# Optimization experiments

Measured on AMD Instinct MI355X. Metric: run time of the kernel, lower is better.

Reference implementation:

```python
import jax, jax.numpy as jnp
import numpy as np

CE_TEMP = 1.0
SIMW_TEMP = 0.1
NSEG = 2048
EPS = 1e-8
NEG = jnp.float32(-1e30)


def setup_inputs() -> dict:
    key = jax.random.key(0)
    k1, k2, k3, k4, k5, k6 = jax.random.split(key, 6)
    N, C, H, W, Ch, S = 2, 19, 128, 128, 256, NSEG
    inputs_plbl = jax.random.normal(k1, (N, C, H, W), dtype=jnp.float32)
    feats_plbl = jax.random.normal(k2, (N, Ch, H, W), dtype=jnp.float32)
    inputs = jax.random.normal(k3, (N, C, H, W), dtype=jnp.float32)
    # multi-hot targets per superpixel; ~2.3 active classes on average -> many multi-hot rows
    targets = jax.random.bernoulli(k4, 0.12, (N, S, C)).astype(jnp.float32)
    superpixels = jax.random.randint(k5, (N, H, W), 0, S, dtype=jnp.int32)
    spmasks = jax.random.bernoulli(k6, 0.5, (N, H, W))
    return {"inputs_plbl": inputs_plbl, "feats_plbl": feats_plbl, "inputs": inputs,
            "targets": targets, "superpixels": superpixels, "spmasks": spmasks}


def _per_image(out_plbl, feat, out, trg_table, sp, mask):
    # out_plbl: [HW,C] softmax'd pseudo-label probs; feat: [HW,Ch]; out: [HW,C];
    # trg_table: [S,C] multi-hot; sp: [HW] int superpixel ids; mask: [HW] bool
    HW, C = out_plbl.shape
    S = trg_table.shape[0]
    trg_pix = trg_table[sp]                                  # [HW,C]
    multi_spx = trg_table.sum(-1) > 1.0                      # [S]
    valid = mask & multi_spx[sp]                             # == spmask & multi-hot mask

    # scatter_max: argmax pixel per (superpixel, class) among valid pixels
    scores = jnp.where(valid[:, None], out_plbl, NEG)
    seg_max = jax.ops.segment_max(scores, sp, num_segments=S)       # [S,C]
    is_max = valid[:, None] & (scores >= seg_max[sp])
    cand = jnp.where(is_max, jnp.arange(HW, dtype=jnp.int32)[:, None], HW)
    proto_idx = jax.ops.segment_min(cand, sp, num_segments=S)       # [S,C]
    proto_idx = jnp.clip(proto_idx, 0, HW - 1)

    # prototype features and per-pixel similarities to own-superpixel class prototypes
    proto_feat = feat[proto_idx]                             # [S,C,Ch]
    pf_pix = proto_feat[sp]                                  # [HW,C,Ch] (dominant intermediate)
    sim = jnp.einsum('kcd,kd->kc', pf_pix, feat) / SIMW_TEMP  # [HW,C]

    # scatter_softmax over the active classes of the pixel's superpixel
    active = trg_pix > 0.0
    w_multi = jax.nn.softmax(jnp.where(active, sim, NEG), axis=-1)
    w_row = jnp.where(active, w_multi, trg_pix)              # inactive entries keep 0
    w = jnp.where(valid[:, None], w_row, trg_pix)            # non-multi pixels keep one-hot
    w = jax.lax.stop_gradient(w)                             # original computes weights under no_grad

    ce = -jnp.log(out + EPS)                                 # [HW,C]
    contrib = jnp.where(mask[:, None], w * ce, 0.0)
    any_valid = jnp.any(valid)                               # image skipped if no multi-hot masked pixel
    loss_i = jnp.where(any_valid, contrib.sum(), 0.0)
    cnt_i = jnp.where(any_valid, mask.sum(), 0)
    return loss_i, cnt_i


def reference(inputs_plbl, feats_plbl, inputs, targets, superpixels, spmasks):
    N, C, H, W = inputs_plbl.shape
    Ch = feats_plbl.shape[1]
    out_plbl = jax.nn.softmax(inputs_plbl / CE_TEMP, axis=1).transpose(0, 2, 3, 1).reshape(N, -1, C)
    feats = feats_plbl.transpose(0, 2, 3, 1).reshape(N, -1, Ch)
    out = jax.nn.softmax(inputs / CE_TEMP, axis=1).transpose(0, 2, 3, 1).reshape(N, -1, C)
    sp = superpixels.reshape(N, -1)
    mask = spmasks.reshape(N, -1)
    loss_i, cnt_i = jax.vmap(_per_image)(out_plbl, feats, out, targets, sp, mask)
    total = loss_i.sum()
    cnt = cnt_i.sum()
    return jnp.where(cnt > 0, total / jnp.maximum(cnt, 1).astype(jnp.float32), 0.0)
```

## Files before the change

kernel.cpp:

```cpp
#include <hip/hip_runtime.h>
#include <cstdint>
#include <cstddef>

#define NN   2
#define CC   19
#define HWD  16384
#define CH   256
#define SS   2048
#define BCAP 32

#define EPSV 1e-8f

__global__ __launch_bounds__(256) void k_main(
        const float* __restrict__ xp, const float* __restrict__ xi,
        const float* __restrict__ trg, const int* __restrict__ sp,
        const int* __restrict__ msk,
        int* __restrict__ sp_cnt, unsigned short* __restrict__ bucket,
        unsigned char* __restrict__ validf, float* __restrict__ plbl_pm,
        float* __restrict__ ce_pm, int* __restrict__ cnt,
        int* __restrict__ vcnt, float* __restrict__ slots) {
    int gid = blockIdx.x * blockDim.x + threadIdx.x;
    int partB = (gid >= NN * HWD);
    int idx = partB ? gid - NN * HWD : gid;
    int n = idx >> 14;
    int k = idx & (HWD - 1);
    int lane = threadIdx.x & 63;
    int m = (msk[idx] != 0);
    int s = sp[idx];
    const float* t = trg + ((size_t)n * SS + s) * CC;
    int mu = 0;
    if (m) {
        float ts = 0.f;
        #pragma unroll
        for (int c = 0; c < CC; ++c) ts += t[c];
        mu = (ts > 1.0f);
    }
    int valid = m && mu;

    if (!partB) {
        validf[idx] = (unsigned char)valid;
        unsigned long long mb = __ballot(m);
        unsigned long long vb = __ballot(valid);
        if (valid) {
            int cell = n * SS + s;
            int pos = atomicAdd(&sp_cnt[cell], 1);
            if (pos < BCAP) bucket[(size_t)cell * BCAP + pos] = (unsigned short)k;
            const float* a = xp + (size_t)n * CC * HWD + k;
            float v[CC];
            float mx = -1e30f;
            #pragma unroll
            for (int c = 0; c < CC; ++c) { v[c] = a[(size_t)c * HWD]; mx = fmaxf(mx, v[c]); }
            float su = 0.f;
            #pragma unroll
            for (int c = 0; c < CC; ++c) { v[c] = expf(v[c] - mx); su += v[c]; }
            float inv = 1.f / su;
            float* op = plbl_pm + (size_t)idx * CC;
            #pragma unroll
            for (int c = 0; c < CC; ++c) op[c] = v[c] * inv;
        }
        if (lane == 0) {
            if (mb) atomicAdd(&cnt[n], __popcll(mb));
            if (vb) atomicAdd(&vcnt[n], __popcll(vb));
        }
    } else {
        float contrib = 0.f;
        if (m) {
            const float* b = xi + (size_t)n * CC * HWD + k;
            float v[CC];
            float mx = -1e30f;
            #pragma unroll
            for (int c = 0; c < CC; ++c) { v[c] = b[(size_t)c * HWD]; mx = fmaxf(mx, v[c]); }
            float su = 0.f;
            #pragma unroll
            for (int c = 0; c < CC; ++c) { v[c] = expf(v[c] - mx); su += v[c]; }
            float inv = 1.f / su;
            if (mu) {
                float* cp = ce_pm + (size_t)idx * CC;
                #pragma unroll
                for (int c = 0; c < CC; ++c) cp[c] = -logf(v[c] * inv + EPSV);
            } else {
                #pragma unroll
                for (int c = 0; c < CC; ++c) contrib += t[c] * (-logf(v[c] * inv + EPSV));
            }
        }
        #pragma unroll
        for (int off = 32; off >= 1; off >>= 1) contrib += __shfl_xor(contrib, off);
        if (lane == 0 && contrib != 0.f)
            atomicAdd(&slots[n * 128 + ((idx >> 6) & 127)], contrib);
    }
}

__global__ void k_transpose(const float* __restrict__ F,
                            const unsigned char* __restrict__ validf,
                            float* __restrict__ FT) {
    __shared__ float tile[64][65];
    __shared__ unsigned char vld[64];
    int n  = blockIdx.z;
    int k0 = blockIdx.x * 64;
    int d0 = blockIdx.y * 64;
    const float* src = F + (size_t)n * CH * HWD;
    float* dst = FT + (size_t)n * HWD * CH;
    int tx = threadIdx.x, ty = threadIdx.y;
    if (ty == 0) vld[tx] = validf[n * HWD + k0 + tx];
    #pragma unroll
    for (int i = 0; i < 16; ++i) {
        int dd = ty + 4 * i;
        tile[dd][tx] = src[(size_t)(d0 + dd) * HWD + (k0 + tx)];
    }
    __syncthreads();
    #pragma unroll
    for (int i = 0; i < 16; ++i) {
        int kk = ty + 4 * i;
        if (vld[kk]) dst[(size_t)(k0 + kk) * CH + (d0 + tx)] = tile[tx][kk];
    }
}

__global__ __launch_bounds__(256) void k_sim(
        const float* __restrict__ feat_t, const float* __restrict__ ce_pm,
        const float* __restrict__ plbl_pm, const float* __restrict__ trg,
        const int* __restrict__ sp_cnt, const unsigned short* __restrict__ bucket,
        float* __restrict__ slots) {
    int id = blockIdx.x;
    int cnt_c = sp_cnt[id];
    if (cnt_c == 0) return;
    cnt_c = min(cnt_c, BCAP);
    int n    = id >> 11;
    int tid  = threadIdx.x;
    int lane = tid & 63;
    int wv   = tid >> 6;

    __shared__ float protoF[CC][CH];
    __shared__ float s_bv[4][CC];
    __shared__ int   s_bi[4][CC];
    __shared__ int   s_proto[CC];
    __shared__ int   actc[CC];

    float t = (lane < CC) ? trg[(size_t)id * CC + lane] : 0.f;
    unsigned long long act = __ballot(t > 0.f);
    int nact = __popcll(act);
    int apos = __popcll(act & ((1ull << lane) - 1ull));
    if ((act >> lane) & 1ull) actc[apos] = lane;
    int mypix = (lane < cnt_c) ? (int)bucket[(size_t)id * BCAP + lane] : 0;

    float bv = -1e30f;
    int   bi = HWD;
    for (int i = wv; i < cnt_c; i += 4) {
        int pix = __shfl(mypix, i);
        if (lane < CC) {
            float v = plbl_pm[((size_t)(n * HWD + pix)) * CC + lane];
            if (v > bv || (v == bv && pix < bi)) { bv = v; bi = pix; }
        }
    }
    if (lane < CC) { s_bv[wv][lane] = bv; s_bi[wv][lane] = bi; }
    __syncthreads();
    if (lane < CC) {
        bv = -1e30f; bi = HWD;
        #pragma unroll
        for (int j = 0; j < 4; ++j) {
            float v = s_bv[j][lane];
            int   p = s_bi[j][lane];
            if (v > bv || (v == bv && p < bi)) { bv = v; bi = p; }
        }
        if ((act >> lane) & 1ull) s_proto[apos] = bi;
    }
    __syncthreads();

    for (int a = wv; a < nact; a += 4) {
        int p = s_proto[a];
        ((float4*)(&protoF[a][0]))[lane] =
            ((const float4*)(feat_t + ((size_t)(n * HWD + p)) * CH))[lane];
    }
    __syncthreads();

    float wcontrib = 0.f;
    for (int i = wv; i < cnt_c; i += 4) {
        int pix = __shfl(mypix, i);
        float ce = (lane < nact)
                 ? ce_pm[((size_t)(n * HWD + pix)) * CC + actc[lane]] : 0.f;
        float4 f = ((const float4*)(feat_t + ((size_t)(n * HWD + pix)) * CH))[lane];
        float mysim = -1e30f;
        for (int a = 0; a < nact; ++a) {
            float4 pf = ((const float4*)(&protoF[a][0]))[lane];
            float d = f.x * pf.x + f.y * pf.y + f.z * pf.z + f.w * pf.w;
            #pragma unroll
            for (int off = 32; off >= 1; off >>= 1) d += __shfl_xor(d, off);
            if (lane == a) mysim = d * 10.0f;
        }
        float mx = mysim;
        #pragma unroll
        for (int off = 32; off >= 1; off >>= 1) mx = fmaxf(mx, __shfl_xor(mx, off));
        float e = (lane < nact) ? expf(mysim - mx) : 0.f;
        float se = e;
        #pragma unroll
        for (int off = 32; off >= 1; off >>= 1) se += __shfl_xor(se, off);
        float c1 = (e / se) * ce;
        #pragma unroll
        for (int off = 32; off >= 1; off >>= 1) c1 += __shfl_xor(c1, off);
        wcontrib += c1;
    }
    if (lane == 0 && wcontrib != 0.f)
        atomicAdd(&slots[n * 128 + (id & 127)], wcontrib);
}

__global__ void k_final(const float* __restrict__ slots, const int* __restrict__ cnt,
                        const int* __restrict__ vcnt, float* __restrict__ out) {
    __shared__ float red[2];
    int t = threadIdx.x;
    int w = t >> 6;
    int lane = t & 63;
    float v = slots[w * 128 + lane] + slots[w * 128 + lane + 64];
    #pragma unroll
    for (int off = 32; off >= 1; off >>= 1) v += __shfl_xor(v, off);
    if (lane == 0) red[w] = v;
    __syncthreads();
    if (t == 0) {
        float total = 0.f;
        int c = 0;
        for (int n = 0; n < NN; ++n)
            if (vcnt[n] > 0) { total += red[n]; c += cnt[n]; }
        out[0] = (c > 0) ? total / (float)c : 0.f;
    }
}

extern "C" void kernel_launch(void* const* d_in, const int* in_sizes, int n_in,
                              void* d_out, int out_size, void* d_ws, size_t ws_size,
                              hipStream_t stream) {
    const float* inputs_plbl = (const float*)d_in[0];
    const float* feats_plbl  = (const float*)d_in[1];
    const float* inputs      = (const float*)d_in[2];
    const float* targets     = (const float*)d_in[3];
    const int*   superpixels = (const int*)d_in[4];
    const int*   spmasks     = (const int*)d_in[5];
    float* out = (float*)d_out;

    char* ws = (char*)d_ws;
    int*   sp_cnt = (int*)ws;
    int*   cnt    = (int*)(ws + 16384);
    int*   vcnt   = (int*)(ws + 16392);
    float* slots  = (float*)(ws + 16416);
    unsigned char*  validf = (unsigned char*)(ws + 17440);
    unsigned short* bucket = (unsigned short*)(ws + 50208);
    float* plbl_pm = (float*)(ws + 312352);
    float* ce_pm   = (float*)(ws + 2802720);
    float* feat_t  = (float*)(ws + 5293088);

    hipMemsetAsync(ws, 0, 17440, stream);

    k_main<<<(2 * NN * HWD) / 256, 256, 0, stream>>>(
        inputs_plbl, inputs, targets, superpixels, spmasks,
        sp_cnt, bucket, validf, plbl_pm, ce_pm, cnt, vcnt, slots);
    dim3 tg(HWD / 64, CH / 64, NN);
    k_transpose<<<tg, dim3(64, 4), 0, stream>>>(feats_plbl, validf, feat_t);
    k_sim<<<NN * SS, 256, 0, stream>>>(feat_t, ce_pm, plbl_pm, targets,
                                       sp_cnt, bucket, slots);
    k_final<<<1, 128, 0, stream>>>(slots, cnt, vcnt, out);
}
```

Baseline: 133.4 us.

## Fuse pixel softmax kernel and feature transpose into one launch

Merges the per-pixel softmax/CE kernel and the masked feature transpose into a single kernel, with blocks partitioned by blockIdx. The transpose blocks now recompute the valid flag from mask, superpixel and target sums, so the validf buffer is gone. This removes one launch and the serial dependency between the two kernels, letting the transpose run alongside the softmax work. The cost is redundant target-row reads in the transpose blocks and a shared-memory tile that every block reserves, including the softmax blocks that never use it.

```diff
diff --git a/kernel.cpp b/kernel.cpp
--- a/kernel.cpp
+++ b/kernel.cpp
@@ -11,107 +11,123 @@
 
 #define EPSV 1e-8f
 
-__global__ __launch_bounds__(256) void k_main(
+#define MAIN_BLKS  (2 * NN * HWD / 256)
+#define TRAN_BLKS  ((HWD / 64) * (CH / 64) * NN)
+
+__global__ __launch_bounds__(256) void k_fused(
         const float* __restrict__ xp, const float* __restrict__ xi,
-        const float* __restrict__ trg, const int* __restrict__ sp,
-        const int* __restrict__ msk,
+        const float* __restrict__ F, const float* __restrict__ trg,
+        const int* __restrict__ sp, const int* __restrict__ msk,
         int* __restrict__ sp_cnt, unsigned short* __restrict__ bucket,
-        unsigned char* __restrict__ validf, float* __restrict__ plbl_pm,
-        float* __restrict__ ce_pm, int* __restrict__ cnt,
+        float* __restrict__ plbl_pm, float* __restrict__ ce_pm,
+        float* __restrict__ feat_t, int* __restrict__ cnt,
         int* __restrict__ vcnt, float* __restrict__ slots) {
-    int gid = blockIdx.x * blockDim.x + threadIdx.x;
-    int partB = (gid >= NN * HWD);
-    int idx = partB ? gid - NN * HWD : gid;
-    int n = idx >> 14;
-    int k = idx & (HWD - 1);
-    int lane = threadIdx.x & 63;
-    int m = (msk[idx] != 0);
-    int s = sp[idx];
-    const float* t = trg + ((size_t)n * SS + s) * CC;
-    int mu = 0;
-    if (m) {
-        float ts = 0.f;
-        #pragma unroll
-        for (int c = 0; c < CC; ++c) ts += t[c];
-        mu = (ts > 1.0f);
-    }
-    int valid = m && mu;
-
-    if (!partB) {
-        validf[idx] = (unsigned char)valid;
-        unsigned long long mb = __ballot(m);
-        unsigned long long vb = __ballot(valid);
-        if (valid) {
-            int cell = n * SS + s;
-            int pos = atomicAdd(&sp_cnt[cell], 1);
-            if (pos < BCAP) bucket[(size_t)cell * BCAP + pos] = (unsigned short)k;
-            const float* a = xp + (size_t)n * CC * HWD + k;
-            float v[CC];
-            float mx = -1e30f;
-            #pragma unroll
-            for (int c = 0; c < CC; ++c) { v[c] = a[(size_t)c * HWD]; mx = fmaxf(mx, v[c]); }
-            float su = 0.f;
-            #pragma unroll
-            for (int c = 0; c < CC; ++c) { v[c] = expf(v[c] - mx); su += v[c]; }
-            float inv = 1.f / su;
-            float* op = plbl_pm + (size_t)idx * CC;
-            #pragma unroll
-            for (int c = 0; c < CC; ++c) op[c] = v[c] * inv;
-        }
-        if (lane == 0) {
-            if (mb) atomicAdd(&cnt[n], __popcll(mb));
-            if (vb) atomicAdd(&vcnt[n], __popcll(vb));
-        }
-    } else {
-        float contrib = 0.f;
-        if (m) {
-            const float* b = xi + (size_t)n * CC * HWD + k;
-            float v[CC];
-            float mx = -1e30f;
-            #pragma unroll
-            for (int c = 0; c < CC; ++c) { v[c] = b[(size_t)c * HWD]; mx = fmaxf(mx, v[c]); }
-            float su = 0.f;
-            #pragma unroll
-            for (int c = 0; c < CC; ++c) { v[c] = expf(v[c] - mx); su += v[c]; }
-            float inv = 1.f / su;
-            if (mu) {
-                float* cp = ce_pm + (size_t)idx * CC;
-                #pragma unroll
-                for (int c = 0; c < CC; ++c) cp[c] = -logf(v[c] * inv + EPSV);
-            } else {
-                #pragma unroll
-                for (int c = 0; c < CC; ++c) contrib += t[c] * (-logf(v[c] * inv + EPSV));
-            }
-        }
-        #pragma unroll
-        for (int off = 32; off >= 1; off >>= 1) contrib += __shfl_xor(contrib, off);
-        if (lane == 0 && contrib != 0.f)
-            atomicAdd(&slots[n * 128 + ((idx >> 6) & 127)], contrib);
-    }
-}
-
-__global__ void k_transpose(const float* __restrict__ F,
-                            const unsigned char* __restrict__ validf,
-                            float* __restrict__ FT) {
     __shared__ float tile[64][65];
     __shared__ unsigned char vld[64];
-    int n  = blockIdx.z;
-    int k0 = blockIdx.x * 64;
-    int d0 = blockIdx.y * 64;
-    const float* src = F + (size_t)n * CH * HWD;
-    float* dst = FT + (size_t)n * HWD * CH;
-    int tx = threadIdx.x, ty = threadIdx.y;
-    if (ty == 0) vld[tx] = validf[n * HWD + k0 + tx];
-    #pragma unroll
-    for (int i = 0; i < 16; ++i) {
-        int dd = ty + 4 * i;
-        tile[dd][tx] = src[(size_t)(d0 + dd) * HWD + (k0 + tx)];
-    }
-    __syncthreads();
-    #pragma unroll
-    for (int i = 0; i < 16; ++i) {
-        int kk = ty + 4 * i;
-        if (vld[kk]) dst[(size_t)(k0 + kk) * CH + (d0 + tx)] = tile[tx][kk];
+
+    if (blockIdx.x < MAIN_BLKS) {
+        int gid = blockIdx.x * blockDim.x + threadIdx.x;
+        int partB = (gid >= NN * HWD);
+        int idx = partB ? gid - NN * HWD : gid;
+        int n = idx >> 14;
+        int k = idx & (HWD - 1);
+        int lane = threadIdx.x & 63;
+        int m = (msk[idx] != 0);
+        int s = sp[idx];
+        const float* t = trg + ((size_t)n * SS + s) * CC;
+        int mu = 0;
+        if (m) {
+            float ts = 0.f;
+            #pragma unroll
+            for (int c = 0; c < CC; ++c) ts += t[c];
+            mu = (ts > 1.0f);
+        }
+        int valid = m && mu;
+
+        if (!partB) {
+            unsigned long long mb = __ballot(m);
+            unsigned long long vb = __ballot(valid);
+            if (valid) {
+                int cell = n * SS + s;
+                int pos = atomicAdd(&sp_cnt[cell], 1);
+                if (pos < BCAP) bucket[(size_t)cell * BCAP + pos] = (unsigned short)k;
+                const float* a = xp + (size_t)n * CC * HWD + k;
+                float v[CC];
+                float mx = -1e30f;
+                #pragma unroll
+                for (int c = 0; c < CC; ++c) { v[c] = a[(size_t)c * HWD]; mx = fmaxf(mx, v[c]); }
+                float su = 0.f;
+                #pragma unroll
+                for (int c = 0; c < CC; ++c) { v[c] = expf(v[c] - mx); su += v[c]; }
+                float inv = 1.f / su;
+                float* op = plbl_pm + (size_t)idx * CC;
+                #pragma unroll
+                for (int c = 0; c < CC; ++c) op[c] = v[c] * inv;
+            }
+            if (lane == 0) {
+                if (mb) atomicAdd(&cnt[n], __popcll(mb));
+                if (vb) atomicAdd(&vcnt[n], __popcll(vb));
+            }
+        } else {
+            float contrib = 0.f;
+            if (m) {
+                const float* b = xi + (size_t)n * CC * HWD + k;
+                float v[CC];
+                float mx = -1e30f;
+                #pragma unroll
+                for (int c = 0; c < CC; ++c) { v[c] = b[(size_t)c * HWD]; mx = fmaxf(mx, v[c]); }
+                float su = 0.f;
+                #pragma unroll
+                for (int c = 0; c < CC; ++c) { v[c] = expf(v[c] - mx); su += v[c]; }
+                float inv = 1.f / su;
+                if (mu) {
+                    float* cp = ce_pm + (size_t)idx * CC;
+                    #pragma unroll
+                    for (int c = 0; c < CC; ++c) cp[c] = -logf(v[c] * inv + EPSV);
+                } else {
+                    #pragma unroll
+                    for (int c = 0; c < CC; ++c) contrib += t[c] * (-logf(v[c] * inv + EPSV));
+                }
+            }
+            #pragma unroll
+            for (int off = 32; off >= 1; off >>= 1) contrib += __shfl_xor(contrib, off);
+            if (lane == 0 && contrib != 0.f)
+                atomicAdd(&slots[n * 128 + ((idx >> 6) & 127)], contrib);
+        }
+    } else {
+        int b2 = blockIdx.x - MAIN_BLKS;
+        int k0 = (b2 & 255) * 64;
+        int d0 = ((b2 >> 8) & 3) * 64;
+        int n  = b2 >> 10;
+        int tx = threadIdx.x & 63, ty = threadIdx.x >> 6;
+        const float* src = F + (size_t)n * CH * HWD;
+        float* dst = feat_t + (size_t)n * HWD * CH;
+
+        if (ty == 0) {
+            int pix = n * HWD + k0 + tx;
+            int m = (msk[pix] != 0);
+            int flag = 0;
+            if (m) {
+                int s = sp[pix];
+                const float* t = trg + ((size_t)n * SS + s) * CC;
+                float ts = 0.f;
+                #pragma unroll
+                for (int c = 0; c < CC; ++c) ts += t[c];
+                flag = (ts > 1.0f);
+            }
+            vld[tx] = (unsigned char)flag;
+        }
+        #pragma unroll
+        for (int i = 0; i < 16; ++i) {
+            int dd = ty + 4 * i;
+            tile[dd][tx] = src[(size_t)(d0 + dd) * HWD + (k0 + tx)];
+        }
+        __syncthreads();
+        #pragma unroll
+        for (int i = 0; i < 16; ++i) {
+            int kk = ty + 4 * i;
+            if (vld[kk]) dst[(size_t)(k0 + kk) * CH + (d0 + tx)] = tile[tx][kk];
+        }
     }
 }
 
@@ -238,19 +254,16 @@
     int*   cnt    = (int*)(ws + 16384);
     int*   vcnt   = (int*)(ws + 16392);
     float* slots  = (float*)(ws + 16416);
-    unsigned char*  validf = (unsigned char*)(ws + 17440);
-    unsigned short* bucket = (unsigned short*)(ws + 50208);
-    float* plbl_pm = (float*)(ws + 312352);
-    float* ce_pm   = (float*)(ws + 2802720);
-    float* feat_t  = (float*)(ws + 5293088);
+    unsigned short* bucket = (unsigned short*)(ws + 17440);
+    float* plbl_pm = (float*)(ws + 279584);
+    float* ce_pm   = (float*)(ws + 2769952);
+    float* feat_t  = (float*)(ws + 5260320);
 
     hipMemsetAsync(ws, 0, 17440, stream);
 
-    k_main<<<(2 * NN * HWD) / 256, 256, 0, stream>>>(
-        inputs_plbl, inputs, targets, superpixels, spmasks,
-        sp_cnt, bucket, validf, plbl_pm, ce_pm, cnt, vcnt, slots);
-    dim3 tg(HWD / 64, CH / 64, NN);
-    k_transpose<<<tg, dim3(64, 4), 0, stream>>>(feats_plbl, validf, feat_t);
+    k_fused<<<MAIN_BLKS + TRAN_BLKS, 256, 0, stream>>>(
+        inputs_plbl, inputs, feats_plbl, targets, superpixels, spmasks,
+        sp_cnt, bucket, plbl_pm, ce_pm, feat_t, cnt, vcnt, slots);
     k_sim<<<NN * SS, 256, 0, stream>>>(feat_t, ce_pm, plbl_pm, targets,
                                        sp_cnt, bucket, slots);
     k_final<<<1, 128, 0, stream>>>(slots, cnt, vcnt, out);
```

New measurement: 128.9 us. 1.03x faster.
